# Kernel tuning notes

Measured on AMD Instinct MI355X. Metric: run time of the kernel, lower is better.

The kernel has to match this reference:

```python
import jax, jax.numpy as jnp
import numpy as np

NUM_ITERATIONS = 3
EPS = 1e-08

def squash(s, axis=-1):
    norm = jnp.linalg.norm(s, axis=axis, keepdims=True)
    scale = norm ** 2 / (1 + norm ** 2)
    return scale * s / (norm + EPS)

def setup_inputs() -> dict:
    key = jax.random.key(0)
    k1, k2 = jax.random.split(key)
    B, C, M, O, I = 256, 1152, 8, 16, 8
    u = jax.random.normal(k1, (B, C, I), dtype=jnp.float32)
    W = jax.random.normal(k2, (C, M, O, I), dtype=jnp.float32)
    return {"u": u, "W": W}

def reference(u, W):
    B, C, I = u.shape
    M, O = W.shape[1], W.shape[2]
    # u_hat: [B, C, M, O] -- predicted output capsule vectors
    u_hat = jnp.einsum('cmoi,bci->bcmo', W, u)
    b = jnp.zeros((B, C, M), dtype=u.dtype)
    v = None
    for r in range(NUM_ITERATIONS):
        c = jax.nn.softmax(b, axis=2)  # softmax over emotion dim
        s = jnp.einsum('bcm,bcmo->bmo', c, u_hat)
        v = squash(s)  # [B, M, O]
        if r < NUM_ITERATIONS - 1:
            uv = jnp.einsum('bcmo,bmo->bcm', u_hat, v)
            b = b + uv
    return v
```

## Files before the change

kernel.cpp:

```cpp
#include <hip/hip_runtime.h>

#define B_SZ 256
#define C_SZ 1152
#define MO   128
#define CSPL 32
#define CRNG (C_SZ / CSPL)
#define CAPS_EPS 1e-8f

struct alignas(8) H4 { _Float16 h[4]; };

__global__ __launch_bounds__(256) void caps_uhat(
    const float* __restrict__ u,
    const float* __restrict__ W,
    H4* __restrict__ uhat,
    float* __restrict__ part0)
{
    const int bt  = blockIdx.x & 31;
    const int csp = blockIdx.x >> 5;
    const int tid = threadIdx.x;
    const int g   = tid >> 5;
    const int l   = tid & 31;
    const int b   = bt * 8 + g;
    const int mo4 = l * 4;

    __shared__ __align__(16) float wT[8][132];

    float acc[4] = {0.f, 0.f, 0.f, 0.f};
    const int cbeg = csp * CRNG, cend = cbeg + CRNG;

    for (int c = cbeg; c < cend; ++c) {
        __syncthreads();
        {
            const float4 wv = *reinterpret_cast<const float4*>(
                W + (size_t)c * 1024 + tid * 4);
            const int mo = tid >> 1, i0 = (tid & 1) * 4;
            wT[i0 + 0][mo] = wv.x; wT[i0 + 1][mo] = wv.y;
            wT[i0 + 2][mo] = wv.z; wT[i0 + 3][mo] = wv.w;
        }
        __syncthreads();

        const float4* up = reinterpret_cast<const float4*>(
            u + ((size_t)b * C_SZ + c) * 8);
        float4 u0 = up[0], u1 = up[1];
        float u8[8] = {u0.x, u0.y, u0.z, u0.w, u1.x, u1.y, u1.z, u1.w};

        float uh[4] = {0.f, 0.f, 0.f, 0.f};
#pragma unroll
        for (int i = 0; i < 8; ++i) {
            float4 w4 = *reinterpret_cast<const float4*>(&wT[i][mo4]);
            uh[0] = fmaf(w4.x, u8[i], uh[0]);
            uh[1] = fmaf(w4.y, u8[i], uh[1]);
            uh[2] = fmaf(w4.z, u8[i], uh[2]);
            uh[3] = fmaf(w4.w, u8[i], uh[3]);
        }
        H4 hv;
        hv.h[0] = (_Float16)uh[0]; hv.h[1] = (_Float16)uh[1];
        hv.h[2] = (_Float16)uh[2]; hv.h[3] = (_Float16)uh[3];
        uhat[((size_t)c * B_SZ + b) * 32 + l] = hv;
#pragma unroll
        for (int j = 0; j < 4; ++j) acc[j] += uh[j];
    }
    *reinterpret_cast<float4*>(part0 + ((size_t)csp * B_SZ + b) * MO + mo4) =
        make_float4(acc[0] * 0.125f, acc[1] * 0.125f,
                    acc[2] * 0.125f, acc[3] * 0.125f);
}

__global__ __launch_bounds__(128) void caps_vcalc(
    const float* __restrict__ part_in,
    const float* __restrict__ addv,
    float* __restrict__ vout)
{
    const int b = blockIdx.x, t = threadIdx.x;
    float s = 0.f;
#pragma unroll
    for (int k = 0; k < CSPL; ++k)
        s += part_in[((size_t)k * B_SZ + b) * MO + t];
    float n2 = s * s;
    n2 += __shfl_xor(n2, 1);
    n2 += __shfl_xor(n2, 2);
    n2 += __shfl_xor(n2, 4);
    n2 += __shfl_xor(n2, 8);
    float norm = sqrtf(n2);
    float v = (n2 / (1.f + n2)) * s / (norm + CAPS_EPS);
    if (addv) v += addv[(size_t)b * MO + t];
    vout[(size_t)b * MO + t] = v;
}

__global__ __launch_bounds__(256) void caps_route(
    const H4* __restrict__ uhat,
    const float* __restrict__ vbuf,
    float* __restrict__ part_out)
{
    const int bt  = blockIdx.x & 31;
    const int csp = blockIdx.x >> 5;
    const int tid = threadIdx.x;
    const int g   = tid >> 5;
    const int l   = tid & 31;
    const int b   = bt * 8 + g;
    const int mo4 = l * 4;

    const float4 v4 = *reinterpret_cast<const float4*>(
        vbuf + (size_t)b * MO + mo4);
    float acc[4] = {0.f, 0.f, 0.f, 0.f};

    const int cbeg = csp * CRNG, cend = cbeg + CRNG;
    const H4* base = uhat + (size_t)b * 32 + l;

    H4 r0 = base[(size_t)cbeg * B_SZ * 32];
    H4 r1 = base[(size_t)(cbeg + 1) * B_SZ * 32];

    for (int c = cbeg; c < cend; c += 2) {
        H4 n0 = r0, n1 = r1;
        if (c + 2 < cend) {
            n0 = base[(size_t)(c + 2) * B_SZ * 32];
            n1 = base[(size_t)(c + 3) * B_SZ * 32];
        }
#pragma unroll
        for (int q = 0; q < 2; ++q) {
            H4 r = q ? r1 : r0;
            float uh0 = (float)r.h[0], uh1 = (float)r.h[1];
            float uh2 = (float)r.h[2], uh3 = (float)r.h[3];
            float uv = uh0 * v4.x + uh1 * v4.y + uh2 * v4.z + uh3 * v4.w;
            uv += __shfl_xor(uv, 1);
            uv += __shfl_xor(uv, 2);
            float mx = fmaxf(uv, __shfl_xor(uv, 4));
            mx = fmaxf(mx, __shfl_xor(mx, 8));
            mx = fmaxf(mx, __shfl_xor(mx, 16));
            float e = expf(uv - mx);
            float den = e;
            den += __shfl_xor(den, 4);
            den += __shfl_xor(den, 8);
            den += __shfl_xor(den, 16);
            float cw = e / den;
            acc[0] = fmaf(cw, uh0, acc[0]);
            acc[1] = fmaf(cw, uh1, acc[1]);
            acc[2] = fmaf(cw, uh2, acc[2]);
            acc[3] = fmaf(cw, uh3, acc[3]);
        }
        r0 = n0; r1 = n1;
    }
    *reinterpret_cast<float4*>(part_out + ((size_t)csp * B_SZ + b) * MO + mo4) =
        make_float4(acc[0], acc[1], acc[2], acc[3]);
}

template <int R>
__global__ __launch_bounds__(256) void caps_small(
    const float* __restrict__ u, const float* __restrict__ W,
    const float* __restrict__ s_in, const float* __restrict__ v0_in,
    float* __restrict__ s_out, float* __restrict__ v0_out,
    float* __restrict__ out)
{
    const int b = blockIdx.x, tid = threadIdx.x;
    __shared__ float sh_v[8][17];
    __shared__ float sh_part[256][17];

    if (R >= 1) {
        if (tid < 128) {
            float val = s_in[b * 128 + tid];
            float n2 = val * val;
            n2 += __shfl_xor(n2, 1); n2 += __shfl_xor(n2, 2);
            n2 += __shfl_xor(n2, 4); n2 += __shfl_xor(n2, 8);
            float norm = sqrtf(n2);
            float v = (n2 / (1.f + n2)) * val / (norm + CAPS_EPS);
            int m = tid >> 4, o = tid & 15;
            if (R == 1) { v0_out[b * 128 + tid] = v; sh_v[m][o] = v; }
            else        { sh_v[m][o] = v + v0_in[b * 128 + tid]; }
        }
        __syncthreads();
    }
    const int c_local = tid >> 3, m = tid & 7;
    float s_acc[16];
#pragma unroll
    for (int o = 0; o < 16; ++o) s_acc[o] = 0.f;
    for (int cc = 0; cc < C_SZ; cc += 32) {
        const int c = cc + c_local;
        const float4* up = reinterpret_cast<const float4*>(
            u + (size_t)(b * C_SZ + c) * 8);
        float4 u0 = up[0], u1 = up[1];
        float u8[8] = {u0.x, u0.y, u0.z, u0.w, u1.x, u1.y, u1.z, u1.w};
        float uh[16];
        const float4* wp = reinterpret_cast<const float4*>(
            W + (size_t)((c * 8 + m) * 16) * 8);
#pragma unroll
        for (int o = 0; o < 16; ++o) {
            float4 w0 = wp[o * 2], w1 = wp[o * 2 + 1];
            uh[o] = w0.x * u8[0] + w0.y * u8[1] + w0.z * u8[2] + w0.w * u8[3] +
                    w1.x * u8[4] + w1.y * u8[5] + w1.z * u8[6] + w1.w * u8[7];
        }
        float cw;
        if (R == 0) cw = 0.125f;
        else {
            float uv = 0.f;
#pragma unroll
            for (int o = 0; o < 16; ++o) uv = fmaf(uh[o], sh_v[m][o], uv);
            float mx = uv;
            mx = fmaxf(mx, __shfl_xor(mx, 1));
            mx = fmaxf(mx, __shfl_xor(mx, 2));
            mx = fmaxf(mx, __shfl_xor(mx, 4));
            float e = expf(uv - mx);
            float den = e;
            den += __shfl_xor(den, 1); den += __shfl_xor(den, 2);
            den += __shfl_xor(den, 4);
            cw = e / den;
        }
#pragma unroll
        for (int o = 0; o < 16; ++o) s_acc[o] = fmaf(cw, uh[o], s_acc[o]);
    }
#pragma unroll
    for (int o = 0; o < 16; ++o) sh_part[tid][o] = s_acc[o];
    __syncthreads();
    if (tid < 128) {
        const int m2 = tid >> 4, o2 = tid & 15;
        float s = 0.f;
#pragma unroll
        for (int gg = 0; gg < 32; ++gg) s += sh_part[gg * 8 + m2][o2];
        if (R < 2) s_out[b * 128 + tid] = s;
        else {
            float n2 = s * s;
            n2 += __shfl_xor(n2, 1); n2 += __shfl_xor(n2, 2);
            n2 += __shfl_xor(n2, 4); n2 += __shfl_xor(n2, 8);
            float norm = sqrtf(n2);
            out[b * 128 + tid] = (n2 / (1.f + n2)) * s / (norm + CAPS_EPS);
        }
    }
}

extern "C" void kernel_launch(void* const* d_in, const int* in_sizes, int n_in,
                              void* d_out, int out_size, void* d_ws, size_t ws_size,
                              hipStream_t stream) {
    const float* u = (const float*)d_in[0];
    const float* W = (const float*)d_in[1];
    float* out = (float*)d_out;

    const size_t UHAT_ELEMS = (size_t)C_SZ * B_SZ * 32;
    const size_t UHAT_BYTES = UHAT_ELEMS * 8;
    const size_t PART_FLOATS = (size_t)CSPL * B_SZ * MO;
    const size_t NEED = UHAT_BYTES + 2 * PART_FLOATS * 4 + 2 * B_SZ * MO * 4;

    if (ws_size >= NEED) {
        H4* uhat     = (H4*)d_ws;
        float* partA = (float*)((char*)d_ws + UHAT_BYTES);
        float* partB = partA + PART_FLOATS;
        float* v0    = partB + PART_FLOATS;
        float* vsum  = v0 + B_SZ * MO;

        dim3 gridC(CSPL * 32), blk(256);
        caps_uhat <<<gridC, blk, 0, stream>>>(u, W, uhat, partA);
        caps_vcalc<<<dim3(B_SZ), dim3(128), 0, stream>>>(partA, nullptr, v0);
        caps_route<<<gridC, blk, 0, stream>>>(uhat, v0, partB);
        caps_vcalc<<<dim3(B_SZ), dim3(128), 0, stream>>>(partB, v0, vsum);
        caps_route<<<gridC, blk, 0, stream>>>(uhat, vsum, partA);
        caps_vcalc<<<dim3(B_SZ), dim3(128), 0, stream>>>(partA, nullptr, out);
    } else {
        float* sA = (float*)d_ws;
        float* sB = sA + 32768;
        float* v0 = sB + 32768;
        dim3 grid(B_SZ), blk(256);
        caps_small<0><<<grid, blk, 0, stream>>>(u, W, nullptr, nullptr, sA, nullptr, nullptr);
        caps_small<1><<<grid, blk, 0, stream>>>(u, W, sA, nullptr, sB, v0, nullptr);
        caps_small<2><<<grid, blk, 0, stream>>>(u, W, sB, v0, nullptr, nullptr, out);
    }
}
```

Before: 79.81 us.

## Restructure uhat kernel per capsule with register-held W and split uniform routing pass

```diff
diff --git a/kernel.cpp b/kernel.cpp
--- a/kernel.cpp
+++ b/kernel.cpp
@@ -8,61 +8,42 @@
 #define CAPS_EPS 1e-8f
 
 struct alignas(8) H4 { _Float16 h[4]; };
+union PK2 { unsigned int u32; _Float16 h[2]; };
 
 __global__ __launch_bounds__(256) void caps_uhat(
     const float* __restrict__ u,
     const float* __restrict__ W,
-    H4* __restrict__ uhat,
-    float* __restrict__ part0)
-{
-    const int bt  = blockIdx.x & 31;
-    const int csp = blockIdx.x >> 5;
-    const int tid = threadIdx.x;
-    const int g   = tid >> 5;
-    const int l   = tid & 31;
-    const int b   = bt * 8 + g;
-    const int mo4 = l * 4;
-
-    __shared__ __align__(16) float wT[8][132];
-
-    float acc[4] = {0.f, 0.f, 0.f, 0.f};
-    const int cbeg = csp * CRNG, cend = cbeg + CRNG;
-
-    for (int c = cbeg; c < cend; ++c) {
-        __syncthreads();
-        {
-            const float4 wv = *reinterpret_cast<const float4*>(
-                W + (size_t)c * 1024 + tid * 4);
-            const int mo = tid >> 1, i0 = (tid & 1) * 4;
-            wT[i0 + 0][mo] = wv.x; wT[i0 + 1][mo] = wv.y;
-            wT[i0 + 2][mo] = wv.z; wT[i0 + 3][mo] = wv.w;
-        }
-        __syncthreads();
-
-        const float4* up = reinterpret_cast<const float4*>(
-            u + ((size_t)b * C_SZ + c) * 8);
-        float4 u0 = up[0], u1 = up[1];
-        float u8[8] = {u0.x, u0.y, u0.z, u0.w, u1.x, u1.y, u1.z, u1.w};
-
-        float uh[4] = {0.f, 0.f, 0.f, 0.f};
-#pragma unroll
-        for (int i = 0; i < 8; ++i) {
-            float4 w4 = *reinterpret_cast<const float4*>(&wT[i][mo4]);
-            uh[0] = fmaf(w4.x, u8[i], uh[0]);
-            uh[1] = fmaf(w4.y, u8[i], uh[1]);
-            uh[2] = fmaf(w4.z, u8[i], uh[2]);
-            uh[3] = fmaf(w4.w, u8[i], uh[3]);
-        }
-        H4 hv;
-        hv.h[0] = (_Float16)uh[0]; hv.h[1] = (_Float16)uh[1];
-        hv.h[2] = (_Float16)uh[2]; hv.h[3] = (_Float16)uh[3];
-        uhat[((size_t)c * B_SZ + b) * 32 + l] = hv;
-#pragma unroll
-        for (int j = 0; j < 4; ++j) acc[j] += uh[j];
-    }
-    *reinterpret_cast<float4*>(part0 + ((size_t)csp * B_SZ + b) * MO + mo4) =
-        make_float4(acc[0] * 0.125f, acc[1] * 0.125f,
-                    acc[2] * 0.125f, acc[3] * 0.125f);
+    unsigned int* __restrict__ uhat)
+{
+    const int bid = blockIdx.x;
+    const int c   = (bid & 7) * 144 + (bid >> 3);
+    const int l   = threadIdx.x & 63;
+    const int wv  = __builtin_amdgcn_readfirstlane(threadIdx.x >> 6);
+
+    const float4* wp =
+        reinterpret_cast<const float4*>(W + (size_t)c * 1024) + l * 4;
+    const float4 wa = wp[0], wb = wp[1], wc4 = wp[2], wd = wp[3];
+
+    unsigned int* ub = uhat + (size_t)c * B_SZ * 64 + l;
+    const int b0 = wv * 64;
+
+    for (int bb = 0; bb < 64; bb += 8) {
+#pragma unroll
+        for (int k = 0; k < 8; ++k) {
+            const int b = b0 + bb + k;
+            const float4* up = reinterpret_cast<const float4*>(
+                u + ((size_t)b * C_SZ + c) * 8);
+            const float4 u0 = up[0], u1 = up[1];
+            float h0 = wa.x*u0.x + wa.y*u0.y + wa.z*u0.z + wa.w*u0.w
+                     + wb.x*u1.x + wb.y*u1.y + wb.z*u1.z + wb.w*u1.w;
+            float h1 = wc4.x*u0.x + wc4.y*u0.y + wc4.z*u0.z + wc4.w*u0.w
+                     + wd.x*u1.x + wd.y*u1.y + wd.z*u1.z + wd.w*u1.w;
+            PK2 pk;
+            pk.h[0] = (_Float16)h0;
+            pk.h[1] = (_Float16)h1;
+            ub[(size_t)b * 64] = pk.u32;
+        }
+    }
 }
 
 __global__ __launch_bounds__(128) void caps_vcalc(
@@ -86,6 +67,7 @@
     vout[(size_t)b * MO + t] = v;
 }
 
+template <bool UNIF>
 __global__ __launch_bounds__(256) void caps_route(
     const H4* __restrict__ uhat,
     const float* __restrict__ vbuf,
@@ -99,8 +81,9 @@
     const int b   = bt * 8 + g;
     const int mo4 = l * 4;
 
-    const float4 v4 = *reinterpret_cast<const float4*>(
-        vbuf + (size_t)b * MO + mo4);
+    float4 v4 = make_float4(0.f, 0.f, 0.f, 0.f);
+    if (!UNIF)
+        v4 = *reinterpret_cast<const float4*>(vbuf + (size_t)b * MO + mo4);
     float acc[4] = {0.f, 0.f, 0.f, 0.f};
 
     const int cbeg = csp * CRNG, cend = cbeg + CRNG;
@@ -120,18 +103,23 @@
             H4 r = q ? r1 : r0;
             float uh0 = (float)r.h[0], uh1 = (float)r.h[1];
             float uh2 = (float)r.h[2], uh3 = (float)r.h[3];
-            float uv = uh0 * v4.x + uh1 * v4.y + uh2 * v4.z + uh3 * v4.w;
-            uv += __shfl_xor(uv, 1);
-            uv += __shfl_xor(uv, 2);
-            float mx = fmaxf(uv, __shfl_xor(uv, 4));
-            mx = fmaxf(mx, __shfl_xor(mx, 8));
-            mx = fmaxf(mx, __shfl_xor(mx, 16));
-            float e = expf(uv - mx);
-            float den = e;
-            den += __shfl_xor(den, 4);
-            den += __shfl_xor(den, 8);
-            den += __shfl_xor(den, 16);
-            float cw = e / den;
+            float cw;
+            if (UNIF) {
+                cw = 0.125f;
+            } else {
+                float uv = uh0 * v4.x + uh1 * v4.y + uh2 * v4.z + uh3 * v4.w;
+                uv += __shfl_xor(uv, 1);
+                uv += __shfl_xor(uv, 2);
+                float mx = fmaxf(uv, __shfl_xor(uv, 4));
+                mx = fmaxf(mx, __shfl_xor(mx, 8));
+                mx = fmaxf(mx, __shfl_xor(mx, 16));
+                float e = expf(uv - mx);
+                float den = e;
+                den += __shfl_xor(den, 4);
+                den += __shfl_xor(den, 8);
+                den += __shfl_xor(den, 16);
+                cw = e / den;
+            }
             acc[0] = fmaf(cw, uh0, acc[0]);
             acc[1] = fmaf(cw, uh1, acc[1]);
             acc[2] = fmaf(cw, uh2, acc[2]);
@@ -232,24 +220,25 @@
     const float* W = (const float*)d_in[1];
     float* out = (float*)d_out;
 
-    const size_t UHAT_ELEMS = (size_t)C_SZ * B_SZ * 32;
-    const size_t UHAT_BYTES = UHAT_ELEMS * 8;
+    const size_t UHAT_BYTES  = (size_t)C_SZ * B_SZ * MO * 2;
     const size_t PART_FLOATS = (size_t)CSPL * B_SZ * MO;
     const size_t NEED = UHAT_BYTES + 2 * PART_FLOATS * 4 + 2 * B_SZ * MO * 4;
 
     if (ws_size >= NEED) {
-        H4* uhat     = (H4*)d_ws;
+        unsigned int* uhat_w = (unsigned int*)d_ws;
+        const H4* uhat_r = (const H4*)d_ws;
         float* partA = (float*)((char*)d_ws + UHAT_BYTES);
         float* partB = partA + PART_FLOATS;
         float* v0    = partB + PART_FLOATS;
         float* vsum  = v0 + B_SZ * MO;
 
-        dim3 gridC(CSPL * 32), blk(256);
-        caps_uhat <<<gridC, blk, 0, stream>>>(u, W, uhat, partA);
+        dim3 gridU(C_SZ), gridR(CSPL * 32), blk(256);
+        caps_uhat<<<gridU, blk, 0, stream>>>(u, W, uhat_w);
+        caps_route<true ><<<gridR, blk, 0, stream>>>(uhat_r, nullptr, partA);
         caps_vcalc<<<dim3(B_SZ), dim3(128), 0, stream>>>(partA, nullptr, v0);
-        caps_route<<<gridC, blk, 0, stream>>>(uhat, v0, partB);
+        caps_route<false><<<gridR, blk, 0, stream>>>(uhat_r, v0, partB);
         caps_vcalc<<<dim3(B_SZ), dim3(128), 0, stream>>>(partB, v0, vsum);
-        caps_route<<<gridC, blk, 0, stream>>>(uhat, vsum, partA);
+        caps_route<false><<<gridR, blk, 0, stream>>>(uhat_r, vsum, partA);
         caps_vcalc<<<dim3(B_SZ), dim3(128), 0, stream>>>(partA, nullptr, out);
     } else {
         float* sA = (float*)d_ws;
```

New measurement: 98.90 us. 23.9% more time.
